# Optimization experiments

Measured on AMD Instinct MI355X. Metric: run time of the kernel, lower is better.

Reference implementation:

```python
import jax, jax.numpy as jnp
import numpy as np

DIM = 1024
NUM_HEADS = 16
HEAD_DIM = DIM // NUM_HEADS
CHUNK = 128
SCALE = HEAD_DIM ** -0.5
RMS_EPS_BIT = 1.1920929e-07  # torch.finfo(float32).eps (nn.RMSNorm default)
RMS_EPS_OUT = 1e-6


def activation_quant(x):
    scale = 127.0 / jnp.clip(jnp.max(jnp.abs(x), axis=-1, keepdims=True), 1e-5)
    return jnp.clip(jnp.round(x * scale), -128, 127) / scale


def weight_quant(w):
    scale = 1.0 / jnp.clip(jnp.mean(jnp.abs(w)), 1e-5)
    return jnp.clip(jnp.round(w * scale), -1, 1) / scale


def bitlinear(x, w, b, norm_w):
    xn = x * jax.lax.rsqrt(jnp.mean(x * x, axis=-1, keepdims=True) + RMS_EPS_BIT) * norm_w
    xq = xn + jax.lax.stop_gradient(activation_quant(xn) - xn)
    wq = w + jax.lax.stop_gradient(weight_quant(w) - w)
    return xq @ wq.T + b


def rms_norm(x, w):
    return x * jax.lax.rsqrt(jnp.mean(x * x, axis=-1, keepdims=True) + RMS_EPS_OUT) * w


def apply_rope(x, cos, sin):
    # x: [B,N,H,D]; cos/sin: [N, D//2]
    B, N, H, D = x.shape
    cos_e = jnp.repeat(cos[:N], 2, axis=-1)[None, :, None, :]  # [1,N,1,D]
    sin_e = jnp.repeat(sin[:N], 2, axis=-1)[None, :, None, :]
    xh = x.reshape(B, N, H, D // 2, 2)
    x_rot = jnp.stack([-xh[..., 1], xh[..., 0]], axis=-1).reshape(B, N, H, D)
    return x * cos_e + x_rot * sin_e


def setup_inputs() -> dict:
    key = jax.random.key(0)
    ks = jax.random.split(key, 8)
    B, N = 2, 8192
    return {
        "x": jax.random.normal(ks[0], (B, N, DIM), jnp.float32),
        "cos": jax.random.uniform(ks[1], (N, HEAD_DIM // 2), jnp.float32),
        "sin": jax.random.uniform(ks[2], (N, HEAD_DIM // 2), jnp.float32),
        "qkv_w": jax.random.normal(ks[3], (3 * DIM, DIM), jnp.float32) * 0.02,
        "qkv_b": jnp.zeros((3 * DIM,), jnp.float32),
        "qkv_nw": jnp.ones((DIM,), jnp.float32),
        "proj_w": jax.random.normal(ks[4], (DIM, DIM), jnp.float32) * 0.02,
        "proj_b": jnp.zeros((DIM,), jnp.float32),
        "proj_nw": jnp.ones((DIM,), jnp.float32),
        "norm_w": jnp.ones((DIM,), jnp.float32),
    }


def lightning_attention(x, cos, sin, qkv_w, qkv_b, qkv_nw, proj_w, proj_b, proj_nw, norm_w):
    B, N, C = x.shape
    qkv = bitlinear(x, qkv_w, qkv_b, qkv_nw).reshape(B, N, 3, NUM_HEADS, HEAD_DIM)
    q, k, v = qkv[:, :, 0], qkv[:, :, 1], qkv[:, :, 2]
    q = apply_rope(q, cos, sin)
    k = apply_rope(k, cos, sin)
    # N chosen as a multiple of CHUNK (pad_len == 0)
    T = N // CHUNK
    # [T, B, chunk, H, Dh]
    qc = jnp.moveaxis(q.reshape(B, T, CHUNK, NUM_HEADS, HEAD_DIM), 1, 0)
    kc = jnp.moveaxis(k.reshape(B, T, CHUNK, NUM_HEADS, HEAD_DIM), 1, 0)
    vc = jnp.moveaxis(v.reshape(B, T, CHUNK, NUM_HEADS, HEAD_DIM), 1, 0)
    causal = jnp.tril(jnp.ones((CHUNK, CHUNK), bool))
    neg_inf = jnp.finfo(x.dtype).min

    def step(kv_state, chunk):
        q_t, k_t, v_t = chunk  # each [B, chunk, H, Dh]
        scores = jnp.einsum('bqhd,bkhd->bhqk', q_t, k_t) * SCALE
        scores = jnp.where(causal, scores, neg_inf)
        attn = jax.nn.softmax(scores, axis=-1)
        o_intra = jnp.einsum('bhqk,bkhd->bqhd', attn, v_t)
        o_inter = jnp.einsum('bqhd,bhde->bqhe', q_t, kv_state)
        kv_new = kv_state + jnp.einsum('bkhd,bkhe->bhde', k_t, v_t)
        return kv_new, o_intra + o_inter

    kv0 = jnp.zeros((B, NUM_HEADS, HEAD_DIM, HEAD_DIM), x.dtype)
    _, out = jax.lax.scan(step, kv0, (qc, kc, vc))  # out: [T,B,chunk,H,Dh]
    out = jnp.moveaxis(out, 0, 1).reshape(B, N, C)
    return bitlinear(rms_norm(out, norm_w), proj_w, proj_b, proj_nw)


def reference(x, cos, sin, qkv_w, qkv_b, qkv_nw, proj_w, proj_b, proj_nw, norm_w):
    return lightning_attention(x, cos, sin, qkv_w, qkv_b, qkv_nw, proj_w, proj_b, proj_nw, norm_w)
```

## Files before the change

### kernel.cpp

```cpp
#include <hip/hip_runtime.h>


typedef unsigned short USH;
typedef __attribute__((ext_vector_type(8))) short short8;
typedef __attribute__((ext_vector_type(4))) float f32x4;
typedef __attribute__((ext_vector_type(4))) USH us4;

__device__ __forceinline__ float b2f(USH u) { return __uint_as_float(((unsigned)u) << 16); }
__device__ __forceinline__ USH f2b(float f) {
    unsigned u = __float_as_uint(f);
    u += 0x7fffu + ((u >> 16) & 1u);
    return (USH)(u >> 16);
}
__device__ __forceinline__ f32x4 mfma16(short8 a, short8 b, f32x4 c) {
    return __builtin_amdgcn_mfma_f32_16x16x32_bf16(a, b, c, 0, 0, 0);
}
__device__ __forceinline__ void gload_lds16(const void* g, void* l) {
    __builtin_amdgcn_global_load_lds(
        (const __attribute__((address_space(1))) unsigned*)g,
        (__attribute__((address_space(3))) unsigned*)l, 16, 0, 0);
}

__device__ __forceinline__ float blk_sum(float v, float* red) {
#pragma unroll
    for (int o = 32; o; o >>= 1) v += __shfl_xor(v, o);
    __syncthreads();
    if ((threadIdx.x & 63) == 0) red[threadIdx.x >> 6] = v;
    __syncthreads();
    return red[0] + red[1] + red[2] + red[3];
}
__device__ __forceinline__ float blk_max(float v, float* red) {
#pragma unroll
    for (int o = 32; o; o >>= 1) v = fmaxf(v, __shfl_xor(v, o));
    __syncthreads();
    if ((threadIdx.x & 63) == 0) red[threadIdx.x >> 6] = v;
    __syncthreads();
    return fmaxf(fmaxf(red[0], red[1]), fmaxf(red[2], red[3]));
}

__global__ __launch_bounds__(256) void k_wabs(const float* __restrict__ qw,
                                              const float* __restrict__ pw,
                                              float* __restrict__ partials) {
    __shared__ float red[4];
    int which = blockIdx.y;
    const float4* p = (const float4*)(which ? pw : qw);
    int n4 = which ? (1024 * 1024 / 4) : (3072 * 1024 / 4);
    float s = 0.f;
    for (int i = blockIdx.x * 256 + threadIdx.x; i < n4; i += 256 * 256) {
        float4 v = p[i];
        s += fabsf(v.x) + fabsf(v.y) + fabsf(v.z) + fabsf(v.w);
    }
#pragma unroll
    for (int o = 32; o; o >>= 1) s += __shfl_xor(s, o);
    if ((threadIdx.x & 63) == 0) red[threadIdx.x >> 6] = s;
    __syncthreads();
    if (threadIdx.x == 0)
        partials[which * 256 + blockIdx.x] = red[0] + red[1] + red[2] + red[3];
}

__global__ __launch_bounds__(256) void k_wsum(const float* __restrict__ partials,
                                              float* __restrict__ sums) {
    __shared__ double red[4];
    int which = blockIdx.x;
    double v = (double)partials[which * 256 + threadIdx.x];
#pragma unroll
    for (int o = 32; o; o >>= 1) v += __shfl_xor(v, o);
    if ((threadIdx.x & 63) == 0) red[threadIdx.x >> 6] = v;
    __syncthreads();
    if (threadIdx.x == 0)
        sums[which] = (float)(red[0] + red[1] + red[2] + red[3]);
}

__global__ __launch_bounds__(256) void k_wquant(const float* __restrict__ qw,
                                                const float* __restrict__ pw,
                                                const float* __restrict__ sums,
                                                USH* __restrict__ wqk, USH* __restrict__ wqp) {
    int id = blockIdx.x * 256 + threadIdx.x;
    float4 v; USH* dst; float sc;
    if (id < 786432) {
        v = ((const float4*)qw)[id];
        sc = 1.f / fmaxf(sums[0] * (1.f / 3145728.f), 1e-5f);
        dst = wqk + (size_t)id * 4;
    } else {
        int j = id - 786432;
        v = ((const float4*)pw)[j];
        sc = 1.f / fmaxf(sums[1] * (1.f / 1048576.f), 1e-5f);
        dst = wqp + (size_t)j * 4;
    }
    us4 o;
    o.x = f2b(fminf(fmaxf(rintf(v.x * sc), -1.f), 1.f));
    o.y = f2b(fminf(fmaxf(rintf(v.y * sc), -1.f), 1.f));
    o.z = f2b(fminf(fmaxf(rintf(v.z * sc), -1.f), 1.f));
    o.w = f2b(fminf(fmaxf(rintf(v.w * sc), -1.f), 1.f));
    *(us4*)dst = o;
}

__global__ __launch_bounds__(256) void k_actq(const float* __restrict__ x,
                                              const float* __restrict__ nw,
                                              USH* __restrict__ xq, float* __restrict__ inva) {
    __shared__ float red[4];
    int row = blockIdx.x, tid = threadIdx.x;
    float4 v = ((const float4*)(x + (size_t)row * 1024))[tid];
    float4 w = ((const float4*)nw)[tid];
    float ss = v.x * v.x + v.y * v.y + v.z * v.z + v.w * v.w;
    ss = blk_sum(ss, red);
    float r1 = rsqrtf(ss * (1.f / 1024.f) + 1.1920929e-07f);
    float x0 = v.x * r1 * w.x, x1 = v.y * r1 * w.y, x2 = v.z * r1 * w.z, x3 = v.w * r1 * w.w;
    float am = fmaxf(fmaxf(fabsf(x0), fabsf(x1)), fmaxf(fabsf(x2), fabsf(x3)));
    am = blk_max(am, red);
    float amc = fmaxf(am, 1e-5f);
    float sc = 127.f / amc;
    us4 o;
    o.x = f2b(fminf(fmaxf(rintf(x0 * sc), -128.f), 127.f));
    o.y = f2b(fminf(fmaxf(rintf(x1 * sc), -128.f), 127.f));
    o.z = f2b(fminf(fmaxf(rintf(x2 * sc), -128.f), 127.f));
    o.w = f2b(fminf(fmaxf(rintf(x3 * sc), -128.f), 127.f));
    *(us4*)(xq + (size_t)row * 1024 + tid * 4) = o;
    if (tid == 0) inva[row] = amc * (1.f / 127.f);
}

__global__ __launch_bounds__(256) void k_norm2q(const USH* __restrict__ oat,
                                                const float* __restrict__ nw,
                                                const float* __restrict__ pnw,
                                                USH* __restrict__ xq, float* __restrict__ inva) {
    __shared__ float red[4];
    int row = blockIdx.x, tid = threadIdx.x;
    us4 ov = *(const us4*)(oat + (size_t)row * 1024 + tid * 4);
    float o0 = b2f(ov.x), o1 = b2f(ov.y), o2 = b2f(ov.z), o3 = b2f(ov.w);
    float4 w = ((const float4*)nw)[tid];
    float4 pw = ((const float4*)pnw)[tid];
    float ss1 = blk_sum(o0 * o0 + o1 * o1 + o2 * o2 + o3 * o3, red);
    float r1 = rsqrtf(ss1 * (1.f / 1024.f) + 1e-6f);
    float y0 = o0 * r1 * w.x, y1 = o1 * r1 * w.y, y2 = o2 * r1 * w.z, y3 = o3 * r1 * w.w;
    float ss2 = blk_sum(y0 * y0 + y1 * y1 + y2 * y2 + y3 * y3, red);
    float r2 = rsqrtf(ss2 * (1.f / 1024.f) + 1.1920929e-07f);
    float z0 = y0 * r2 * pw.x, z1 = y1 * r2 * pw.y, z2 = y2 * r2 * pw.z, z3 = y3 * r2 * pw.w;
    float am = fmaxf(fmaxf(fabsf(z0), fabsf(z1)), fmaxf(fabsf(z2), fabsf(z3)));
    am = blk_max(am, red);
    float amc = fmaxf(am, 1e-5f);
    float sc = 127.f / amc;
    us4 q;
    q.x = f2b(fminf(fmaxf(rintf(z0 * sc), -128.f), 127.f));
    q.y = f2b(fminf(fmaxf(rintf(z1 * sc), -128.f), 127.f));
    q.z = f2b(fminf(fmaxf(rintf(z2 * sc), -128.f), 127.f));
    q.w = f2b(fminf(fmaxf(rintf(z3 * sc), -128.f), 127.f));
    *(us4*)(xq + (size_t)row * 1024 + tid * 4) = q;
    if (tid == 0) inva[row] = amc * (1.f / 127.f);
}

template <bool OUT_BF16>
__global__ __launch_bounds__(512, 2) void k_gemm(const USH* __restrict__ A, const USH* __restrict__ W,
                                                 const float* __restrict__ inva,
                                                 const float* __restrict__ wsum, float wcnt,
                                                 const float* __restrict__ bias,
                                                 void* __restrict__ out, int Nn, int K) {
    __shared__ __align__(16) USH lds[3 * 16384];
    const int tid = threadIdx.x;
    const int wv = tid >> 6, lane = tid & 63, quad = lane >> 4, lid = lane & 15;
    const int wr = wv >> 2, wc = wv & 3;

    const int nbn = gridDim.x;
    const int nwg = nbn * gridDim.y;
    const int bid = blockIdx.y * nbn + blockIdx.x;
    const int swb = (bid & 7) * (nwg >> 3) + (bid >> 3);
    const int bn = swb % nbn, bm = swb / nbn;

    const int T = K >> 5;

    const USH* ag[2]; const USH* wg[2];
#pragma unroll
    for (int j = 0; j < 2; j++) {
        int r = (j * 8 + wv) * 16 + (lane >> 2);
        int sw = (r & 3) ^ ((r >> 2) & 1);
        int c16 = (lane & 3) ^ sw;
        ag[j] = A + (size_t)(bm * 256 + r) * K + c16 * 8;
        wg[j] = W + (size_t)(bn * 256 + r) * K + c16 * 8;
    }
    const int sq = quad ^ ((lid & 3) ^ ((lid >> 2) & 1));
    const int arow = (wr * 128 + lid) * 32 + sq * 8;
    const int brow = (wc * 64 + lid) * 32 + sq * 8;

    f32x4 acc[8][4];
#pragma unroll
    for (int mt = 0; mt < 8; mt++)
#pragma unroll
        for (int nt = 0; nt < 4; nt++)
#pragma unroll
            for (int r = 0; r < 4; r++) acc[mt][nt][r] = 0.f;

#pragma unroll
    for (int t = 0; t < 2; t++) {
        USH* dst = &lds[t * 16384];
#pragma unroll
        for (int j = 0; j < 2; j++) {
            gload_lds16(ag[j] + t * 32, &dst[(j * 8 + wv) * 512]);
            gload_lds16(wg[j] + t * 32, &dst[8192 + (j * 8 + wv) * 512]);
        }
    }

    for (int t = 0; t < T; ++t) {
        const USH* As = &lds[(t % 3) * 16384];
        const USH* Bs = As + 8192;
        USH* Pd = &lds[((t + 2) % 3) * 16384];
        short8 af[8], bf[4];
        if (t + 1 < T) asm volatile("s_waitcnt vmcnt(4) lgkmcnt(0)" ::: "memory");
        else           asm volatile("s_waitcnt vmcnt(0) lgkmcnt(0)" ::: "memory");
        __builtin_amdgcn_s_barrier();
        __builtin_amdgcn_sched_barrier(0);
        asm volatile("" ::: "memory");
        if (t + 2 < T) {
#pragma unroll
            for (int j = 0; j < 2; j++) {
                gload_lds16(ag[j] + (t + 2) * 32, &Pd[(j * 8 + wv) * 512]);
                gload_lds16(wg[j] + (t + 2) * 32, &Pd[8192 + (j * 8 + wv) * 512]);
            }
        }
#pragma unroll
        for (int mt = 0; mt < 8; mt++)
            af[mt] = *(const short8*)&As[arow + mt * 512];
#pragma unroll
        for (int nt = 0; nt < 4; nt++)
            bf[nt] = *(const short8*)&Bs[brow + nt * 512];
        __builtin_amdgcn_s_setprio(1);
#pragma unroll
        for (int mt = 0; mt < 8; mt++)
#pragma unroll
            for (int nt = 0; nt < 4; nt++) acc[mt][nt] = mfma16(af[mt], bf[nt], acc[mt][nt]);
        __builtin_amdgcn_s_setprio(0);
    }

    float wm = fmaxf(wsum[0] * (1.f / wcnt), 1e-5f);
#pragma unroll
    for (int mt = 0; mt < 8; mt++)
#pragma unroll
        for (int r = 0; r < 4; r++) {
            int rowg = bm * 256 + wr * 128 + mt * 16 + quad * 4 + r;
            float ia = inva[rowg] * wm;
#pragma unroll
            for (int nt = 0; nt < 4; nt++) {
                int colg = bn * 256 + wc * 64 + nt * 16 + lid;
                float v = acc[mt][nt][r] * ia + bias[colg];
                if (OUT_BF16) ((USH*)out)[(size_t)rowg * Nn + colg] = f2b(v);
                else ((float*)out)[(size_t)rowg * Nn + colg] = v;
            }
        }
}

__global__ __launch_bounds__(256) void k_rope(USH* __restrict__ qkv,
                                              const float* __restrict__ cs,
                                              const float* __restrict__ sn) {
    int id = blockIdx.x * 256 + threadIdx.x;
    int rowm = id >> 10, p = id & 1023;
    int part = p >> 9, pi = p & 511;
    int h = pi >> 5, i = pi & 31;
    int n = rowm & 8191;
    size_t a = (size_t)rowm * 3072 + part * 1024 + h * 64 + 2 * i;
    float c = cs[n * 32 + i], s = sn[n * 32 + i];
    unsigned* pp = (unsigned*)(qkv + a);
    unsigned u = *pp;
    float x0 = b2f((USH)(u & 0xffff)), x1 = b2f((USH)(u >> 16));
    float y0 = x0 * c - x1 * s;
    float y1 = x1 * c + x0 * s;
    *pp = (unsigned)f2b(y0) | ((unsigned)f2b(y1) << 16);
}

__global__ __launch_bounds__(256) void k_attn_intra(const USH* __restrict__ qkv,
                                                    USH* __restrict__ oat) {
    __shared__ char smem[36864 + 17408];
    USH* qs = (USH*)smem;
    USH* kqs = qs + 128 * 72;
    USH* Ps = (USH*)smem;
    USH* vt = (USH*)(smem + 36864);
    int tid = threadIdx.x, wv = tid >> 6, lane = tid & 63, quad = lane >> 4, lid = lane & 15;
    int t = blockIdx.x, bh = blockIdx.y, b = bh >> 4, h = bh & 15;
    size_t base = ((size_t)(b * 8192 + t * 128)) * 3072 + h * 64;
    int r0 = tid >> 3, c0 = (tid & 7) * 8;
#pragma unroll
    for (int i = 0; i < 4; i++) {
        int r = i * 32 + r0;
        short8 qv = *(const short8*)(qkv + base + (size_t)r * 3072 + c0);
        short8 kv = *(const short8*)(qkv + base + (size_t)r * 3072 + 1024 + c0);
        short8 vv = *(const short8*)(qkv + base + (size_t)r * 3072 + 2048 + c0);
        *(short8*)&qs[r * 72 + c0] = qv;
        *(short8*)&kqs[r * 72 + c0] = kv;
        USH tmp[8]; *(short8*)tmp = vv;
#pragma unroll
        for (int j = 0; j < 8; j++) vt[(c0 + j) * 136 + r] = tmp[j];
    }
    __syncthreads();

    f32x4 accs[2][8];
#pragma unroll
    for (int mt = 0; mt < 2; mt++)
#pragma unroll
        for (int nt = 0; nt < 8; nt++)
#pragma unroll
            for (int r = 0; r < 4; r++) accs[mt][nt][r] = 0.f;
    int R = wv * 32;
#pragma unroll
    for (int ksx = 0; ksx < 2; ksx++) {
        int co = ksx * 32 + quad * 8;
        short8 af0 = *(const short8*)&qs[(R + lid) * 72 + co];
        short8 af1 = *(const short8*)&qs[(R + 16 + lid) * 72 + co];
        short8 bf[8];
#pragma unroll
        for (int nt = 0; nt < 8; nt++) bf[nt] = *(const short8*)&kqs[(nt * 16 + lid) * 72 + co];
#pragma unroll
        for (int nt = 0; nt < 8; nt++) {
            accs[0][nt] = mfma16(af0, bf[nt], accs[0][nt]);
            accs[1][nt] = mfma16(af1, bf[nt], accs[1][nt]);
        }
    }
#pragma unroll
    for (int mt = 0; mt < 2; mt++)
#pragma unroll
        for (int r = 0; r < 4; r++) {
            int row = R + mt * 16 + quad * 4 + r;
            float sv[8];
            float mx = -3.0e38f;
#pragma unroll
            for (int nt = 0; nt < 8; nt++) {
                int col = nt * 16 + lid;
                float v = accs[mt][nt][r] * 0.125f;
                sv[nt] = (col <= row) ? v : -3.0e38f;
                mx = fmaxf(mx, sv[nt]);
            }
#pragma unroll
            for (int o = 8; o; o >>= 1) mx = fmaxf(mx, __shfl_xor(mx, o));
            float sm = 0.f;
#pragma unroll
            for (int nt = 0; nt < 8; nt++) {
                float e = (sv[nt] > -1.0e38f) ? __expf(sv[nt] - mx) : 0.f;
                sv[nt] = e; sm += e;
            }
#pragma unroll
            for (int o = 8; o; o >>= 1) sm += __shfl_xor(sm, o);
            float inv = 1.f / sm;
#pragma unroll
            for (int nt = 0; nt < 8; nt++) accs[mt][nt][r] = sv[nt] * inv;
        }
    __syncthreads();
#pragma unroll
    for (int mt = 0; mt < 2; mt++)
#pragma unroll
        for (int nt = 0; nt < 8; nt++)
#pragma unroll
            for (int r = 0; r < 4; r++)
                Ps[(R + mt * 16 + quad * 4 + r) * 136 + nt * 16 + lid] = f2b(accs[mt][nt][r]);
    __syncthreads();

    f32x4 acco[8];
#pragma unroll
    for (int nt = 0; nt < 8; nt++)
#pragma unroll
        for (int r = 0; r < 4; r++) acco[nt][r] = 0.f;
#pragma unroll
    for (int kq = 0; kq < 4; kq++) {
        int co = kq * 32 + quad * 8;
        short8 av = *(const short8*)&vt[(wv * 16 + lid) * 136 + co];
#pragma unroll
        for (int nt = 0; nt < 8; nt++) {
            short8 bp = *(const short8*)&Ps[(nt * 16 + lid) * 136 + co];
            acco[nt] = mfma16(av, bp, acco[nt]);
        }
    }
    size_t obase = (size_t)(b * 8192 + t * 128) * 1024 + h * 64;
#pragma unroll
    for (int nt = 0; nt < 8; nt++)
#pragma unroll
        for (int r = 0; r < 4; r++) {
            int d = wv * 16 + quad * 4 + r;
            int q = nt * 16 + lid;
            oat[obase + (size_t)q * 1024 + d] = f2b(acco[nt][r]);
        }
}

__global__ __launch_bounds__(256) void k_kvchunk(const USH* __restrict__ qkv,
                                                 float* __restrict__ kvc) {
    __shared__ char smem[2 * 17408];
    USH* kt = (USH*)smem;
    USH* vt = (USH*)(smem + 17408);
    int tid = threadIdx.x, wv = tid >> 6, lane = tid & 63, quad = lane >> 4, lid = lane & 15;
    int t = blockIdx.x, bh = blockIdx.y, b = bh >> 4, h = bh & 15;
    size_t base = ((size_t)(b * 8192 + t * 128)) * 3072 + h * 64;
    int r0 = tid >> 3, c0 = (tid & 7) * 8;
#pragma unroll
    for (int i = 0; i < 4; i++) {
        int r = i * 32 + r0;
        short8 kv = *(const short8*)(qkv + base + (size_t)r * 3072 + 1024 + c0);
        short8 vv = *(const short8*)(qkv + base + (size_t)r * 3072 + 2048 + c0);
        USH tk[8]; *(short8*)tk = kv;
        USH tv[8]; *(short8*)tv = vv;
#pragma unroll
        for (int j = 0; j < 8; j++) {
            kt[(c0 + j) * 136 + r] = tk[j];
            vt[(c0 + j) * 136 + r] = tv[j];
        }
    }
    __syncthreads();
    f32x4 acc[4];
#pragma unroll
    for (int nt = 0; nt < 4; nt++)
#pragma unroll
        for (int r = 0; r < 4; r++) acc[nt][r] = 0.f;
#pragma unroll
    for (int kq = 0; kq < 4; kq++) {
        int co = kq * 32 + quad * 8;
        short8 ak = *(const short8*)&kt[(wv * 16 + lid) * 136 + co];
#pragma unroll
        for (int nt = 0; nt < 4; nt++) {
            short8 bv = *(const short8*)&vt[(nt * 16 + lid) * 136 + co];
            acc[nt] = mfma16(ak, bv, acc[nt]);
        }
    }
    float* out = kvc + ((size_t)bh * 64 + t) * 4096;
#pragma unroll
    for (int nt = 0; nt < 4; nt++)
#pragma unroll
        for (int r = 0; r < 4; r++) {
            int d = wv * 16 + quad * 4 + r, e = nt * 16 + lid;
            out[d * 64 + e] = acc[nt][r];
        }
}

__global__ __launch_bounds__(256) void k_prefix(float* __restrict__ kvc) {
    int gid = blockIdx.x * 256 + threadIdx.x;
    int bh = gid >> 12, idx = gid & 4095;
    float* p = kvc + (size_t)bh * 64 * 4096 + idx;
    float a = 0.f;
    for (int t = 0; t < 64; t++) {
        float c = p[(size_t)t * 4096];
        p[(size_t)t * 4096] = a;
        a += c;
    }
}

__global__ __launch_bounds__(256) void k_ointer(const USH* __restrict__ qkv,
                                                const float* __restrict__ kvc,
                                                USH* __restrict__ oat) {
    __shared__ char smem[18432 + 9216];
    USH* qs = (USH*)smem;
    USH* kvt = (USH*)(smem + 18432);
    int tid = threadIdx.x, wv = tid >> 6, lane = tid & 63, quad = lane >> 4, lid = lane & 15;
    int t = blockIdx.x, bh = blockIdx.y, b = bh >> 4, h = bh & 15;
    size_t base = ((size_t)(b * 8192 + t * 128)) * 3072 + h * 64;
    int r0 = tid >> 3, c0 = (tid & 7) * 8;
#pragma unroll
    for (int i = 0; i < 4; i++) {
        int r = i * 32 + r0;
        short8 qv = *(const short8*)(qkv + base + (size_t)r * 3072 + c0);
        *(short8*)&qs[r * 72 + c0] = qv;
    }
    const float* kv = kvc + ((size_t)bh * 64 + t) * 4096;
#pragma unroll
    for (int j = 0; j < 16; j++) {
        int idx = j * 256 + tid;
        int d = idx >> 6, e = idx & 63;
        kvt[e * 72 + d] = f2b(kv[idx]);
    }
    __syncthreads();
    f32x4 acc[2][4];
#pragma unroll
    for (int mt = 0; mt < 2; mt++)
#pragma unroll
        for (int nt = 0; nt < 4; nt++)
#pragma unroll
            for (int r = 0; r < 4; r++) acc[mt][nt][r] = 0.f;
    int R = wv * 32;
#pragma unroll
    for (int kd = 0; kd < 2; kd++) {
        int co = kd * 32 + quad * 8;
        short8 a0 = *(const short8*)&qs[(R + lid) * 72 + co];
        short8 a1 = *(const short8*)&qs[(R + 16 + lid) * 72 + co];
#pragma unroll
        for (int nt = 0; nt < 4; nt++) {
            short8 bv = *(const short8*)&kvt[(nt * 16 + lid) * 72 + co];
            acc[0][nt] = mfma16(a0, bv, acc[0][nt]);
            acc[1][nt] = mfma16(a1, bv, acc[1][nt]);
        }
    }
#pragma unroll
    for (int mt = 0; mt < 2; mt++)
#pragma unroll
        for (int nt = 0; nt < 4; nt++)
#pragma unroll
            for (int r = 0; r < 4; r++) {
                int row = t * 128 + R + mt * 16 + quad * 4 + r;
                size_t idx = ((size_t)b * 8192 + row) * 1024 + h * 64 + nt * 16 + lid;
                float prev = b2f(oat[idx]);
                oat[idx] = f2b(prev + acc[mt][nt][r]);
            }
}

extern "C" void kernel_launch(void* const* d_in, const int* in_sizes, int n_in,
                              void* d_out, int out_size, void* d_ws, size_t ws_size,
                              hipStream_t stream) {
    const float* x      = (const float*)d_in[0];
    const float* cosp   = (const float*)d_in[1];
    const float* sinp   = (const float*)d_in[2];
    const float* qkv_w  = (const float*)d_in[3];
    const float* qkv_b  = (const float*)d_in[4];
    const float* qkv_nw = (const float*)d_in[5];
    const float* proj_w = (const float*)d_in[6];
    const float* proj_b = (const float*)d_in[7];
    const float* proj_nw= (const float*)d_in[8];
    const float* norm_w = (const float*)d_in[9];
    float* out = (float*)d_out;

    char* w = (char*)d_ws;
    float* sums    = (float*)(w + 0);
    float* partials= (float*)(w + 64);
    USH*   wq_qkv  = (USH*)(w + 4096);
    USH*   wq_proj = (USH*)(w + 4096 + 6291456);
    float* inva    = (float*)(w + 8392704);
    char*  R1      = w + 8458240;
    char*  R2      = w + 8458240 + 33554432;
    USH*   qkv     = (USH*)(w + 8458240 + 2ull * 33554432);
    USH*   xq      = (USH*)R1;
    USH*   oat     = (USH*)R1;
    float* kvc     = (float*)R2;
    USH*   xq2     = (USH*)R2;

    k_wabs<<<dim3(256, 2), 256, 0, stream>>>(qkv_w, proj_w, partials);
    k_wsum<<<2, 256, 0, stream>>>(partials, sums);
    k_wquant<<<4096, 256, 0, stream>>>(qkv_w, proj_w, sums, wq_qkv, wq_proj);
    k_actq<<<16384, 256, 0, stream>>>(x, qkv_nw, xq, inva);
    k_gemm<true><<<dim3(12, 64), 512, 0, stream>>>(xq, wq_qkv, inva, &sums[0], 3145728.f,
                                                   qkv_b, (void*)qkv, 3072, 1024);
    k_rope<<<65536, 256, 0, stream>>>(qkv, cosp, sinp);
    k_attn_intra<<<dim3(64, 32), 256, 0, stream>>>(qkv, oat);
    k_kvchunk<<<dim3(64, 32), 256, 0, stream>>>(qkv, kvc);
    k_prefix<<<512, 256, 0, stream>>>(kvc);
    k_ointer<<<dim3(64, 32), 256, 0, stream>>>(qkv, kvc, oat);
    k_norm2q<<<16384, 256, 0, stream>>>(oat, norm_w, proj_nw, xq2, inva);
    k_gemm<false><<<dim3(4, 64), 512, 0, stream>>>(xq2, wq_proj, inva, &sums[1], 1048576.f,
                                                   proj_b, (void*)out, 1024, 1024);
    (void)in_sizes; (void)n_in; (void)out_size; (void)ws_size;
}
```

Before: 445.5 us.

## Register double-buffer GEMM fragments and deepen LDS prefetch to three stages

```diff
diff --git a/kernel.cpp b/kernel.cpp
--- a/kernel.cpp
+++ b/kernel.cpp
@@ -167,15 +167,13 @@
 
     const int T = K >> 5;
 
-    const USH* ag[2]; const USH* wg[2];
-#pragma unroll
-    for (int j = 0; j < 2; j++) {
-        int r = (j * 8 + wv) * 16 + (lane >> 2);
-        int sw = (r & 3) ^ ((r >> 2) & 1);
-        int c16 = (lane & 3) ^ sw;
-        ag[j] = A + (size_t)(bm * 256 + r) * K + c16 * 8;
-        wg[j] = W + (size_t)(bn * 256 + r) * K + c16 * 8;
-    }
+    const int r0s = wv * 16 + (lane >> 2);
+    const int sw0 = (r0s & 3) ^ ((r0s >> 2) & 1);
+    const int c0s = ((lane & 3) ^ sw0) * 8;
+    const USH* ag0 = A + (size_t)(bm * 256 + r0s) * K + c0s;
+    const USH* wg0 = W + (size_t)(bn * 256 + r0s) * K + c0s;
+    const size_t J1 = (size_t)128 * K;
+
     const int sq = quad ^ ((lid & 3) ^ ((lid >> 2) & 1));
     const int arow = (wr * 128 + lid) * 32 + sq * 8;
     const int brow = (wc * 64 + lid) * 32 + sq * 8;
@@ -189,45 +187,59 @@
             for (int r = 0; r < 4; r++) acc[mt][nt][r] = 0.f;
 
 #pragma unroll
-    for (int t = 0; t < 2; t++) {
+    for (int t = 0; t < 3; t++) {
         USH* dst = &lds[t * 16384];
-#pragma unroll
-        for (int j = 0; j < 2; j++) {
-            gload_lds16(ag[j] + t * 32, &dst[(j * 8 + wv) * 512]);
-            gload_lds16(wg[j] + t * 32, &dst[8192 + (j * 8 + wv) * 512]);
-        }
-    }
-
-    for (int t = 0; t < T; ++t) {
-        const USH* As = &lds[(t % 3) * 16384];
-        const USH* Bs = As + 8192;
-        USH* Pd = &lds[((t + 2) % 3) * 16384];
-        short8 af[8], bf[4];
-        if (t + 1 < T) asm volatile("s_waitcnt vmcnt(4) lgkmcnt(0)" ::: "memory");
-        else           asm volatile("s_waitcnt vmcnt(0) lgkmcnt(0)" ::: "memory");
-        __builtin_amdgcn_s_barrier();
-        __builtin_amdgcn_sched_barrier(0);
-        asm volatile("" ::: "memory");
-        if (t + 2 < T) {
-#pragma unroll
-            for (int j = 0; j < 2; j++) {
-                gload_lds16(ag[j] + (t + 2) * 32, &Pd[(j * 8 + wv) * 512]);
-                gload_lds16(wg[j] + (t + 2) * 32, &Pd[8192 + (j * 8 + wv) * 512]);
-            }
-        }
-#pragma unroll
-        for (int mt = 0; mt < 8; mt++)
-            af[mt] = *(const short8*)&As[arow + mt * 512];
-#pragma unroll
-        for (int nt = 0; nt < 4; nt++)
-            bf[nt] = *(const short8*)&Bs[brow + nt * 512];
-        __builtin_amdgcn_s_setprio(1);
-#pragma unroll
-        for (int mt = 0; mt < 8; mt++)
-#pragma unroll
-            for (int nt = 0; nt < 4; nt++) acc[mt][nt] = mfma16(af[mt], bf[nt], acc[mt][nt]);
-        __builtin_amdgcn_s_setprio(0);
-    }
+        gload_lds16(ag0 + t * 32,      &dst[wv * 512]);
+        gload_lds16(ag0 + J1 + t * 32, &dst[(8 + wv) * 512]);
+        gload_lds16(wg0 + t * 32,      &dst[8192 + wv * 512]);
+        gload_lds16(wg0 + J1 + t * 32, &dst[8192 + (8 + wv) * 512]);
+    }
+    asm volatile("s_waitcnt vmcnt(8)" ::: "memory");
+    __builtin_amdgcn_s_barrier();
+    __builtin_amdgcn_sched_barrier(0);
+
+    short8 afA[8], bfA[4], afB[8], bfB[4];
+#pragma unroll
+    for (int mt = 0; mt < 8; mt++) afA[mt] = *(const short8*)&lds[arow + mt * 512];
+#pragma unroll
+    for (int nt = 0; nt < 4; nt++) bfA[nt] = *(const short8*)&lds[8192 + brow + nt * 512];
+
+#define GITER(t, afC, bfC, afN, bfN)                                              \
+    do {                                                                          \
+        const USH* Rd = &lds[(((t) + 1) % 3) * 16384];                            \
+        USH* Sd = &lds[((t) % 3) * 16384];                                        \
+        if ((t) + 2 < T) asm volatile("s_waitcnt vmcnt(4) lgkmcnt(0)" ::: "memory"); \
+        else             asm volatile("s_waitcnt vmcnt(0) lgkmcnt(0)" ::: "memory"); \
+        __builtin_amdgcn_s_barrier();                                             \
+        __builtin_amdgcn_sched_barrier(0);                                        \
+        if ((t) + 3 < T) {                                                        \
+            gload_lds16(ag0 + ((t) + 3) * 32,      &Sd[wv * 512]);                \
+            gload_lds16(ag0 + J1 + ((t) + 3) * 32, &Sd[(8 + wv) * 512]);          \
+            gload_lds16(wg0 + ((t) + 3) * 32,      &Sd[8192 + wv * 512]);         \
+            gload_lds16(wg0 + J1 + ((t) + 3) * 32, &Sd[8192 + (8 + wv) * 512]);   \
+        }                                                                         \
+        if ((t) + 1 < T) {                                                        \
+            _Pragma("unroll")                                                     \
+            for (int mt_ = 0; mt_ < 8; mt_++)                                     \
+                afN[mt_] = *(const short8*)&Rd[arow + mt_ * 512];                 \
+            _Pragma("unroll")                                                     \
+            for (int nt_ = 0; nt_ < 4; nt_++)                                     \
+                bfN[nt_] = *(const short8*)&Rd[8192 + brow + nt_ * 512];          \
+        }                                                                         \
+        __builtin_amdgcn_s_setprio(1);                                            \
+        _Pragma("unroll")                                                         \
+        for (int mt_ = 0; mt_ < 8; mt_++)                                         \
+            _Pragma("unroll")                                                     \
+            for (int nt_ = 0; nt_ < 4; nt_++)                                     \
+                acc[mt_][nt_] = mfma16(afC[mt_], bfC[nt_], acc[mt_][nt_]);        \
+        __builtin_amdgcn_s_setprio(0);                                            \
+    } while (0)
+
+    for (int tt = 0; tt < T; tt += 2) {
+        GITER(tt,     afA, bfA, afB, bfB);
+        GITER(tt + 1, afB, bfB, afA, bfA);
+    }
+#undef GITER
 
     float wm = fmaxf(wsum[0] * (1.f / wcnt), 1e-5f);
 #pragma unroll
```

Result: no change. 445.8 us (+0.1%).
